# Optimization experiments

Measured on AMD Instinct MI355X. Metric: run time of the kernel, lower is better.

## Reference

```python
import jax, jax.numpy as jnp
import numpy as np

OC, IC, KH, KW = 256, 128, 3, 3          # conv_weights_shape
S, R, Q = 16, 16, 16                      # n_subspaces, rank_transformations, rank_subspace
CTX = 256
HD, WD = OC * KH, IC * KW                 # dynamic_weights_shape = [768, 384]
ASYM = 1e-3
B = 32


def _make_index():
    # Faithful vectorization of DynamicConv2DMobius._create_index for the
    # non-inverted case (HD > WD): block_id = bi*nbj + bj over 3x3 tiles of the
    # [HD, WD] grid; tile goes to (out = block_id % OC, in = block_id // OC).
    base = np.arange(HD * WD).reshape(HD, WD)
    nbi, nbj = HD // KH, WD // KW          # == OC, IC here
    blocks = base.reshape(nbi, KH, nbj, KW).transpose(0, 2, 1, 3).reshape(nbi * nbj, KH, KW)
    # index[o, i] = blocks[i*OC + o]
    index = blocks.reshape(IC, OC, KH, KW).transpose(1, 0, 2, 3)
    return index.reshape(-1).astype(np.int32)  # flat gather map: conv.flat = dw.flat[idx]


def setup_inputs() -> dict:
    key = jax.random.key(0)
    ks = jax.random.split(key, 12)
    bconv_bound = 1.0 / np.sqrt(IC * KH * KW)
    return {
        "x": jax.random.normal(ks[0], (B, IC, 64, 64), jnp.float32),
        "context": jax.random.normal(ks[1], (B, CTX), jnp.float32),
        "W_mob": jax.random.normal(ks[2], (CTX, S, R, 8), jnp.float32) * 0.05,
        "z": jax.random.normal(ks[3], (S, R, 2), jnp.float32),
        "A_re": jax.random.normal(ks[4], (S, R, Q), jnp.float32) * 0.1,
        "A_im": jax.random.normal(ks[5], (S, R, Q), jnp.float32) * 0.1,
        "U": jax.random.normal(ks[6], (S, HD, Q), jnp.float32) * 0.05,
        "V": jax.random.normal(ks[7], (S, Q, WD), jnp.float32) * 0.05,
        "bias_dw": jax.random.uniform(ks[8], (HD, WD), jnp.float32, -ASYM, ASYM),
        "bias_conv": jax.random.uniform(ks[9], (OC,), jnp.float32, -bconv_bound, bconv_bound),
        "pad_val": jax.random.normal(ks[10], (1,), jnp.float32) * 1e-3,
        "offset_val": jax.random.normal(ks[11], (1,), jnp.float32) * 1e-3,
        "dw_index": jnp.asarray(_make_index()),
    }


def _forward(x, context, W_mob, z, A_re, A_im, U, V, bias_dw, bias_conv,
             pad_val, offset_val, dw_index):
    b = x.shape[0]
    # --- TensorComposerMobius: context -> per-sample Mobius coeffs -> low-rank weights
    m = jnp.einsum('bc,csrk->bsrk', context, W_mob)            # [B,S,R,8]
    a_re, a_im, b_re, b_im, c_re, c_im, d_re, d_im = [m[..., i] for i in range(8)]
    z_re, z_im = z[..., 0], z[..., 1]                           # [S,R]
    num_re = a_re * z_re - a_im * z_im + b_re
    num_im = a_re * z_im + a_im * z_re + b_im
    den_re = c_re * z_re - c_im * z_im + d_re
    den_im = c_re * z_im + c_im * z_re + d_im
    den2 = den_re * den_re + den_im * den_im + ASYM             # asymmetry regularizer
    w_re = (num_re * den_re + num_im * den_im) / den2
    w_im = (num_im * den_re - num_re * den_im) / den2
    s = jnp.einsum('bsr,srq->bsq', w_re, A_re) + jnp.einsum('bsr,srq->bsq', w_im, A_im)
    dw = jnp.einsum('bsq,shq,sqw->bhw', s, U, V)                # [B, 768, 384]
    dw = dw + bias_dw[None]                                     # bias_dynamic_weights_lib
    # --- block-gather into conv weight layout (torch.take with shifted index)
    conv_w = jnp.take(dw.reshape(b, -1), dw_index, axis=1).reshape(b, OC, IC, KH, KW)
    # --- dynamic padding value + dynamic offset
    xo = x + offset_val[0]
    hp, wp = x.shape[2] + 2, x.shape[3] + 2                     # padding [1,1,1,1]
    xp = jnp.full((b, IC, hp, wp), pad_val[0], x.dtype).at[:, :, 1:-1, 1:-1].set(xo)
    # --- per-sample conv2d (batched weights)
    def conv_one(xi, wi):
        return jax.lax.conv_general_dilated(
            xi[None], wi, window_strides=(1, 1), padding='VALID',
            rhs_dilation=(1, 1), dimension_numbers=('NCHW', 'OIHW', 'NCHW'))[0]
    out = jax.vmap(conv_one)(xp, conv_w)                        # [B, OC, 64, 64]
    return out + bias_conv[None, :, None, None]


def reference(x, context, W_mob, z, A_re, A_im, U, V, bias_dw, bias_conv,
              pad_val, offset_val, dw_index):
    return _forward(x, context, W_mob, z, A_re, A_im, U, V, bias_dw, bias_conv,
                    pad_val, offset_val, dw_index)
```

## Files before the change

kernel.cpp:

```cpp
#include <hip/hip_runtime.h>
#include <hip/hip_bf16.h>

typedef __attribute__((ext_vector_type(8))) short short8;
typedef __attribute__((ext_vector_type(4))) float f32x4;
typedef unsigned short u16;

#define B_      32
#define IC_     128
#define OC_     256
#define HD_     768
#define WD_     384
#define CTX_    256

static __device__ __forceinline__ u16 f2bf(float f) {
    union { float f; unsigned u; } x; x.f = f;
    unsigned r = x.u + 0x7FFFu + ((x.u >> 16) & 1u);
    return (u16)(r >> 16);
}

__global__ __launch_bounds__(256) void k1_mobius(
    const float* __restrict__ ctx, const float* __restrict__ Wm,
    const float* __restrict__ z, const float* __restrict__ Are,
    const float* __restrict__ Aim, float* __restrict__ sc) {
    int b = blockIdx.x, t = threadIdx.x;
    __shared__ float lctx[CTX_];
    __shared__ float lwre[256], lwim[256];
    lctx[t] = ctx[b * CTX_ + t];
    __syncthreads();
    float m0=0,m1=0,m2=0,m3=0,m4=0,m5=0,m6=0,m7=0;
    const float* wp = Wm + (size_t)t * 8;
    for (int c = 0; c < CTX_; ++c) {
        const float* w = wp + (size_t)c * 2048;
        float cv = lctx[c];
        m0 += cv*w[0]; m1 += cv*w[1]; m2 += cv*w[2]; m3 += cv*w[3];
        m4 += cv*w[4]; m5 += cv*w[5]; m6 += cv*w[6]; m7 += cv*w[7];
    }
    float zre = z[t*2], zim = z[t*2+1];
    float nre = m0*zre - m1*zim + m2;
    float nim = m0*zim + m1*zre + m3;
    float dre = m4*zre - m5*zim + m6;
    float dim_ = m4*zim + m5*zre + m7;
    float den2 = dre*dre + dim_*dim_ + 1e-3f;
    lwre[t] = (nre*dre + nim*dim_) / den2;
    lwim[t] = (nim*dre - nre*dim_) / den2;
    __syncthreads();
    int s = t >> 4, q = t & 15;
    float acc = 0.f;
    #pragma unroll
    for (int r2 = 0; r2 < 16; ++r2) {
        int sr = s*16 + r2;
        acc += lwre[sr]*Are[sr*16 + q] + lwim[sr]*Aim[sr*16 + q];
    }
    sc[b*256 + t] = acc;
}

__global__ __launch_bounds__(256) void k2_pad(
    const float* __restrict__ x, const float* __restrict__ padv,
    const float* __restrict__ offv, u16* __restrict__ xp) {
    int yy = blockIdx.x, b = blockIdx.y, t = threadIdx.x;
    __shared__ u16 lds[64 * 136];
    float off = offv[0];
    u16 pb = f2bf(padv[0]);
    unsigned pp = (unsigned)pb | ((unsigned)pb << 16);
    int4 padvec = make_int4((int)pp, (int)pp, (int)pp, (int)pp);
    u16* row = xp + (size_t)(b * 66 + yy) * (66 * 128);
    if (yy == 0 || yy == 65) {
        for (int c = t; c < 1056; c += 256)
            *(int4*)(row + c * 8) = padvec;
        return;
    }
    int y = yy - 1;
    const float* xin = x + (size_t)b * 524288 + (size_t)y * 64;
    for (int id = t; id < 8192; id += 256) {
        int i = id >> 6, xx = id & 63;
        lds[xx * 136 + i] = f2bf(xin[(size_t)i * 4096 + xx] + off);
    }
    __syncthreads();
    for (int c = t; c < 1056; c += 256) {
        int e = c * 8, xx = e >> 7, i0 = e & 127;
        int4 v;
        if (xx == 0 || xx == 65) v = padvec;
        else v = *(const int4*)(lds + (xx - 1) * 136 + i0);
        *(int4*)(row + e) = v;
    }
}

__global__ __launch_bounds__(256) void k3a_ucat(
    const float* __restrict__ U, u16* __restrict__ Ucat) {
    int id = blockIdx.x * 256 + threadIdx.x;
    int h = id >> 8, k = id & 255;
    int s = k >> 4, q = k & 15;
    Ucat[id] = f2bf(U[((size_t)s * HD_ + h) * 16 + q]);
}

__global__ __launch_bounds__(256) void k3v_vt(
    const float* __restrict__ V, float* __restrict__ Vt) {
    int id = blockIdx.x * 256 + threadIdx.x;
    int w = id >> 8, k = id & 255;
    Vt[id] = V[(size_t)k * WD_ + w];
}

__global__ __launch_bounds__(256, 2) void k4_dw(
    const u16* __restrict__ Ucat, const float* __restrict__ Vt,
    const float* __restrict__ sc, const float* __restrict__ bias_dw,
    u16* __restrict__ cw2) {
    int mt = blockIdx.x, khkw = blockIdx.y, b = blockIdx.z;
    int kh = khkw / 3, kw = khkw - kh * 3;
    int t = threadIdx.x;
    __shared__ __align__(16) u16 Al[128 * 40];
    __shared__ __align__(16) u16 Bl[128 * 40];
    __shared__ float scl[256];
    scl[t] = sc[b * 256 + t];
    f32x4 acc[4][4] = {};
    int wid = t >> 6, l = t & 63;
    int wm = wid >> 1, wn = wid & 1;
    int lr = l & 15, lg = l >> 4;
    int bi0 = mt * 128;
    for (int kc = 0; kc < 8; ++kc) {
        __syncthreads();
        #pragma unroll
        for (int it = 0; it < 2; ++it) {
            int cid = t + it * 256;
            int g = cid & 3, rr = cid >> 2;
            int4 v = *(const int4*)(Ucat + (size_t)((bi0 + rr) * 3 + kh) * 256 + kc * 32 + g * 8);
            *(int4*)(Al + rr * 40 + g * 8) = v;
        }
        #pragma unroll
        for (int it = 0; it < 4; ++it) {
            int cid = t + it * 256;
            int q = cid & 7, rr = cid >> 3;
            int kb = kc * 32 + q * 4;
            float4 v = *(const float4*)(Vt + (size_t)(rr * 3 + kw) * 256 + kb);
            ushort4 p;
            p.x = f2bf(v.x * scl[kb]);
            p.y = f2bf(v.y * scl[kb + 1]);
            p.z = f2bf(v.z * scl[kb + 2]);
            p.w = f2bf(v.w * scl[kb + 3]);
            *(ushort4*)(Bl + rr * 40 + q * 4) = p;
        }
        __syncthreads();
        short8 a[4];
        #pragma unroll
        for (int fm = 0; fm < 4; ++fm)
            a[fm] = *(const short8*)(Al + (wm * 64 + fm * 16 + lr) * 40 + lg * 8);
        #pragma unroll
        for (int fn = 0; fn < 4; ++fn) {
            short8 bb = *(const short8*)(Bl + (wn * 64 + fn * 16 + lr) * 40 + lg * 8);
            #pragma unroll
            for (int fm = 0; fm < 4; ++fm)
                acc[fm][fn] = __builtin_amdgcn_mfma_f32_16x16x32_bf16(a[fm], bb, acc[fm][fn], 0, 0, 0);
        }
    }
    u16* cwb = cw2 + (size_t)b * 294912;
    #pragma unroll
    for (int fm = 0; fm < 4; ++fm) {
        int i2 = mt * 8 + wm * 4 + fm;
        int B0 = bi0 + wm * 64 + fm * 16 + lg * 4;
        #pragma unroll
        for (int fn = 0; fn < 4; ++fn) {
            int bjj = wn * 64 + fn * 16 + lr;
            int wcol = bjj * 3 + kw;
            float v0 = acc[fm][fn][0] + bias_dw[(B0 + 0) * 3 * 384 + kh * 384 + wcol];
            float v2 = acc[fm][fn][2] + bias_dw[(B0 + 2) * 3 * 384 + kh * 384 + wcol];
            unsigned pe = (unsigned)f2bf(v0) | ((unsigned)f2bf(v2) << 16);
            size_t base = ((size_t)(khkw * 16 + i2) * 256);
            *(unsigned*)(cwb + (base + bjj) * 8 + 2 * lg) = pe;
            float v1 = acc[fm][fn][1] + bias_dw[(B0 + 1) * 3 * 384 + kh * 384 + wcol];
            float v3 = acc[fm][fn][3] + bias_dw[(B0 + 3) * 3 * 384 + kh * 384 + wcol];
            unsigned po = (unsigned)f2bf(v1) | ((unsigned)f2bf(v3) << 16);
            *(unsigned*)(cwb + (base + bjj + 128) * 8 + 2 * lg) = po;
        }
    }
}

__global__ __launch_bounds__(256, 2) void k6_conv(
    const u16* __restrict__ xp, const u16* __restrict__ cw2,
    const float* __restrict__ bias_conv, float* __restrict__ out) {
    int f = blockIdx.x;
    int xcd = f & 7, sub = f >> 3;
    int b = xcd * 4 + (sub >> 5);
    int nt = sub & 31;
    int t = threadIdx.x;
    int y0 = nt * 2;
    __shared__ __align__(16) u16 Xl[4 * 66 * 32];
    f32x4 acc[4][8] = {};
    int wid = t >> 6, l = t & 63, lr = l & 15, lg = l >> 4;
    const u16* xpb = xp + (size_t)b * (66 * 66 * 128);
    const u16* cwb = cw2 + (size_t)b * 294912;
    for (int ic = 0; ic < 4; ++ic) {
        __syncthreads();
        #pragma unroll
        for (int it = 0; it < 5; ++it) {
            int cid = t + it * 256;
            if (cid < 1056) {
                int row = cid / 264, rem = cid - row * 264;
                int col = rem >> 2, g = rem & 3;
                int4 v = *(const int4*)(xpb + ((size_t)((y0 + row) * 66 + col)) * 128 + ic * 32 + g * 8);
                int chunk = (((row * 66 + col) * 4 + g) ^ (col & 7));
                *(int4*)((char*)Xl + chunk * 16) = v;
            }
        }
        __syncthreads();
        #pragma unroll
        for (int khkw = 0; khkw < 9; ++khkw) {
            const int kh = khkw / 3, kw = khkw - kh * 3;
            short8 a[4];
            #pragma unroll
            for (int fm = 0; fm < 4; ++fm) {
                int o = wid * 64 + fm * 16 + lr;
                a[fm] = *(const short8*)(cwb + ((size_t)((khkw * 16 + ic * 4 + lg) * 256 + o) << 3));
            }
            __builtin_amdgcn_s_setprio(1);
            #pragma unroll
            for (int fn = 0; fn < 8; ++fn) {
                int r = (fn >> 2) + kh, c = (fn & 3) * 16 + lr + kw;
                int chunk = (((r * 66 + c) * 4 + lg) ^ (c & 7));
                short8 bb = *(const short8*)((const char*)Xl + chunk * 16);
                #pragma unroll
                for (int fm = 0; fm < 4; ++fm)
                    acc[fm][fn] = __builtin_amdgcn_mfma_f32_16x16x32_bf16(a[fm], bb, acc[fm][fn], 0, 0, 0);
            }
            __builtin_amdgcn_s_setprio(0);
        }
    }
    #pragma unroll
    for (int fm = 0; fm < 4; ++fm)
        #pragma unroll
        for (int fn = 0; fn < 8; ++fn) {
            int y = y0 + (fn >> 2);
            int xb = (fn & 3) * 16 + lr;
            #pragma unroll
            for (int j = 0; j < 4; ++j) {
                int o = wid * 64 + fm * 16 + lg * 4 + j;
                out[(((size_t)b * 256 + o) * 64 + y) * 64 + xb] = acc[fm][fn][j] + bias_conv[o];
            }
        }
}

extern "C" void kernel_launch(void* const* d_in, const int* in_sizes, int n_in,
                              void* d_out, int out_size, void* d_ws, size_t ws_size,
                              hipStream_t stream) {
    const float* x     = (const float*)d_in[0];
    const float* ctx   = (const float*)d_in[1];
    const float* Wm    = (const float*)d_in[2];
    const float* z     = (const float*)d_in[3];
    const float* Are   = (const float*)d_in[4];
    const float* Aim   = (const float*)d_in[5];
    const float* U     = (const float*)d_in[6];
    const float* V     = (const float*)d_in[7];
    const float* bdw   = (const float*)d_in[8];
    const float* bconv = (const float*)d_in[9];
    const float* padv  = (const float*)d_in[10];
    const float* offv  = (const float*)d_in[11];
    float* out = (float*)d_out;
    char* ws = (char*)d_ws;

    u16*   xp   = (u16*)(ws);
    u16*   cw2  = (u16*)(ws + 35684352);
    u16*   Ucat = (u16*)(ws + 54558720);
    float* Vt   = (float*)(ws + 54951936);
    float* sc   = (float*)(ws + 55345152);

    k1_mobius<<<32, 256, 0, stream>>>(ctx, Wm, z, Are, Aim, sc);
    k2_pad<<<dim3(66, 32), 256, 0, stream>>>(x, padv, offv, xp);
    k3a_ucat<<<768, 256, 0, stream>>>(U, Ucat);
    k3v_vt<<<384, 256, 0, stream>>>(V, Vt);
    k4_dw<<<dim3(2, 9, 32), 256, 0, stream>>>(Ucat, Vt, sc, bdw, cw2);
    k6_conv<<<1024, 256, 0, stream>>>(xp, cw2, bconv, out);
}
```

Measured before the change: 368.3 us.

## Double-buffer conv weights and input tiles in LDS via async global-to-LDS loads

The conv kernel now stages both the per-step weight slice and the input row tile into double-buffered LDS with global_load_lds. Waits use explicit vmcnt counts so the next slice's loads overlap the current MFMA step, replacing direct global weight reads and synchronous input staging. The prep kernels for U and V are merged into one launch, and the Mobius context loop now uses float4 loads. The change adds more barriers per step and relies on hand-tuned vmcnt values and an XOR-swizzled LDS layout that must match the address math.

```diff
diff --git a/kernel.cpp b/kernel.cpp
--- a/kernel.cpp
+++ b/kernel.cpp
@@ -16,6 +16,19 @@
     union { float f; unsigned u; } x; x.f = f;
     unsigned r = x.u + 0x7FFFu + ((x.u >> 16) & 1u);
     return (u16)(r >> 16);
+}
+
+static __device__ __forceinline__ void glds16(const void* g, void* l) {
+    __builtin_amdgcn_global_load_lds(
+        (const __attribute__((address_space(1))) unsigned*)g,
+        (__attribute__((address_space(3))) unsigned*)l, 16, 0, 0);
+}
+
+#define BARRIER() asm volatile("s_barrier" ::: "memory")
+template <int N> static __device__ __forceinline__ void waitvm() {
+    if constexpr (N == 0)      asm volatile("s_waitcnt vmcnt(0)" ::: "memory");
+    else if constexpr (N == 4) asm volatile("s_waitcnt vmcnt(4)" ::: "memory");
+    else if constexpr (N == 9) asm volatile("s_waitcnt vmcnt(9)" ::: "memory");
 }
 
 __global__ __launch_bounds__(256) void k1_mobius(
@@ -28,12 +41,14 @@
     lctx[t] = ctx[b * CTX_ + t];
     __syncthreads();
     float m0=0,m1=0,m2=0,m3=0,m4=0,m5=0,m6=0,m7=0;
-    const float* wp = Wm + (size_t)t * 8;
+    const float4* wp4 = (const float4*)Wm + (size_t)t * 2;
+    #pragma unroll 4
     for (int c = 0; c < CTX_; ++c) {
-        const float* w = wp + (size_t)c * 2048;
+        float4 w0 = wp4[(size_t)c * 512];
+        float4 w1 = wp4[(size_t)c * 512 + 1];
         float cv = lctx[c];
-        m0 += cv*w[0]; m1 += cv*w[1]; m2 += cv*w[2]; m3 += cv*w[3];
-        m4 += cv*w[4]; m5 += cv*w[5]; m6 += cv*w[6]; m7 += cv*w[7];
+        m0 += cv*w0.x; m1 += cv*w0.y; m2 += cv*w0.z; m3 += cv*w0.w;
+        m4 += cv*w1.x; m5 += cv*w1.y; m6 += cv*w1.z; m7 += cv*w1.w;
     }
     float zre = z[t*2], zim = z[t*2+1];
     float nre = m0*zre - m1*zim + m2;
@@ -85,19 +100,19 @@
     }
 }
 
-__global__ __launch_bounds__(256) void k3a_ucat(
-    const float* __restrict__ U, u16* __restrict__ Ucat) {
+__global__ __launch_bounds__(256) void k3_prep(
+    const float* __restrict__ U, const float* __restrict__ V,
+    u16* __restrict__ Ucat, float* __restrict__ Vt) {
     int id = blockIdx.x * 256 + threadIdx.x;
-    int h = id >> 8, k = id & 255;
-    int s = k >> 4, q = k & 15;
-    Ucat[id] = f2bf(U[((size_t)s * HD_ + h) * 16 + q]);
-}
-
-__global__ __launch_bounds__(256) void k3v_vt(
-    const float* __restrict__ V, float* __restrict__ Vt) {
-    int id = blockIdx.x * 256 + threadIdx.x;
-    int w = id >> 8, k = id & 255;
-    Vt[id] = V[(size_t)k * WD_ + w];
+    if (id < 768 * 256) {
+        int h = id >> 8, k = id & 255;
+        int s = k >> 4, q = k & 15;
+        Ucat[id] = f2bf(U[((size_t)s * HD_ + h) * 16 + q]);
+    } else {
+        int id2 = id - 768 * 256;
+        int w = id2 >> 8, k = id2 & 255;
+        Vt[id2] = V[(size_t)k * WD_ + w];
+    }
 }
 
 __global__ __launch_bounds__(256, 2) void k4_dw(
@@ -173,6 +188,38 @@
     }
 }
 
+static __device__ __forceinline__ void stage_W(
+    const u16* cwb, int khkw, int ic, u16* wl, int t) {
+    const u16* slice = cwb + ((size_t)(khkw * 16 + ic * 4) * 256) * 8;
+    int wbase = t & ~63;
+    #pragma unroll
+    for (int it = 0; it < 4; ++it) {
+        int cid = it * 256 + t;
+        glds16(slice + (size_t)cid * 8, wl + (size_t)(it * 256 + wbase) * 8);
+    }
+}
+
+static __device__ __forceinline__ void stage_X(
+    const u16* xpb, int ic, int y0, u16* xl, int t) {
+    int wbase = t & ~63;
+    #pragma unroll
+    for (int it = 0; it < 5; ++it) {
+        int cid = it * 256 + t;
+        const u16* g;
+        if (cid < 1056) {
+            int n = cid ^ ((cid >> 3) & 7);
+            int gq = (n >= 792) ? 3 : (n >= 528) ? 2 : (n >= 264) ? 1 : 0;
+            int rem = n - gq * 264;
+            int r = (rem * 993) >> 16;
+            int c = rem - r * 66;
+            g = xpb + ((size_t)(y0 + r) * 66 + c) * 128 + ic * 32 + gq * 8;
+        } else {
+            g = xpb;
+        }
+        glds16(g, xl + (size_t)(it * 256 + wbase) * 8);
+    }
+}
+
 __global__ __launch_bounds__(256, 2) void k6_conv(
     const u16* __restrict__ xp, const u16* __restrict__ cw2,
     const float* __restrict__ bias_conv, float* __restrict__ out) {
@@ -182,45 +229,55 @@
     int nt = sub & 31;
     int t = threadIdx.x;
     int y0 = nt * 2;
-    __shared__ __align__(16) u16 Xl[4 * 66 * 32];
+    __shared__ __align__(16) u16 Wl[2][1024 * 8];
+    __shared__ __align__(16) u16 Xl[2][1280 * 8];
     f32x4 acc[4][8] = {};
     int wid = t >> 6, l = t & 63, lr = l & 15, lg = l >> 4;
     const u16* xpb = xp + (size_t)b * (66 * 66 * 128);
     const u16* cwb = cw2 + (size_t)b * 294912;
+
+    stage_X(xpb, 0, y0, Xl[0], t);
+    stage_W(cwb, 0, 0, Wl[0], t);
+    waitvm<0>();
+    BARRIER();
+
+    #pragma unroll
     for (int ic = 0; ic < 4; ++ic) {
-        __syncthreads();
-        #pragma unroll
-        for (int it = 0; it < 5; ++it) {
-            int cid = t + it * 256;
-            if (cid < 1056) {
-                int row = cid / 264, rem = cid - row * 264;
-                int col = rem >> 2, g = rem & 3;
-                int4 v = *(const int4*)(xpb + ((size_t)((y0 + row) * 66 + col)) * 128 + ic * 32 + g * 8);
-                int chunk = (((row * 66 + col) * 4 + g) ^ (col & 7));
-                *(int4*)((char*)Xl + chunk * 16) = v;
+        #pragma unroll
+        for (int khkw = 0; khkw < 9; ++khkw) {
+            const int s = ic * 9 + khkw;
+            const int kh = khkw / 3, kw = khkw - kh * 3;
+            if (khkw == 8 && ic < 3)
+                stage_X(xpb, ic + 1, y0, Xl[(ic + 1) & 1], t);
+            if (s + 1 < 36) {
+                const int nk = (s + 1) % 9, nic = (s + 1) / 9;
+                stage_W(cwb, nk, nic, Wl[(s + 1) & 1], t);
             }
-        }
-        __syncthreads();
-        #pragma unroll
-        for (int khkw = 0; khkw < 9; ++khkw) {
-            const int kh = khkw / 3, kw = khkw - kh * 3;
+            if (s == 35) waitvm<0>();
+            else if (khkw == 8) waitvm<9>();
+            else waitvm<4>();
+            BARRIER();
+            const u16* wl = Wl[s & 1];
+            const u16* xl = Xl[ic & 1];
             short8 a[4];
             #pragma unroll
             for (int fm = 0; fm < 4; ++fm) {
                 int o = wid * 64 + fm * 16 + lr;
-                a[fm] = *(const short8*)(cwb + ((size_t)((khkw * 16 + ic * 4 + lg) * 256 + o) << 3));
+                a[fm] = *(const short8*)(wl + (size_t)(lg * 256 + o) * 8);
             }
             __builtin_amdgcn_s_setprio(1);
             #pragma unroll
             for (int fn = 0; fn < 8; ++fn) {
                 int r = (fn >> 2) + kh, c = (fn & 3) * 16 + lr + kw;
-                int chunk = (((r * 66 + c) * 4 + lg) ^ (c & 7));
-                short8 bb = *(const short8*)((const char*)Xl + chunk * 16);
+                int n = lg * 264 + r * 66 + c;
+                int m = n ^ ((n >> 3) & 7);
+                short8 bb = *(const short8*)(xl + (size_t)m * 8);
                 #pragma unroll
                 for (int fm = 0; fm < 4; ++fm)
                     acc[fm][fn] = __builtin_amdgcn_mfma_f32_16x16x32_bf16(a[fm], bb, acc[fm][fn], 0, 0, 0);
             }
             __builtin_amdgcn_s_setprio(0);
+            if (s != 35) BARRIER();
         }
     }
     #pragma unroll
@@ -263,8 +320,7 @@
 
     k1_mobius<<<32, 256, 0, stream>>>(ctx, Wm, z, Are, Aim, sc);
     k2_pad<<<dim3(66, 32), 256, 0, stream>>>(x, padv, offv, xp);
-    k3a_ucat<<<768, 256, 0, stream>>>(U, Ucat);
-    k3v_vt<<<384, 256, 0, stream>>>(V, Vt);
+    k3_prep<<<1152, 256, 0, stream>>>(U, V, Ucat, Vt);
     k4_dw<<<dim3(2, 9, 32), 256, 0, stream>>>(Ucat, Vt, sc, bdw, cw2);
     k6_conv<<<1024, 256, 0, stream>>>(xp, cw2, bconv, out);
 }
```

After: 350.0 us. 1.05x faster.
